# Kernel tuning notes

Hardware: AMD Instinct MI355X
Metric: run time of the kernel (lower is better)

## Reference

```python
import jax, jax.numpy as jnp
import numpy as np

N_HEAD = 16
N_EMBD = 1024
D_HEAD = N_EMBD // N_HEAD


def setup_inputs() -> dict:
    key = jax.random.key(0)
    ks = jax.random.split(key, 5)
    B, T, C = 4, 2048, N_EMBD
    s = 1.0 / np.sqrt(C)
    return {
        "x": jax.random.normal(ks[0], (B, T, C), dtype=jnp.float32),
        "w_qkv": jax.random.normal(ks[1], (C, 3 * C), dtype=jnp.float32) * s,
        "b_qkv": jnp.zeros((3 * C,), dtype=jnp.float32),
        "w_out": jax.random.normal(ks[2], (C, C), dtype=jnp.float32) * s,
        "b_out": jnp.zeros((C,), dtype=jnp.float32),
    }


def reference(x, w_qkv, b_qkv, w_out, b_out):
    B, T, C = x.shape
    qkv = x @ w_qkv + b_qkv  # [B,T,3C]
    q, k, v = jnp.split(qkv, 3, axis=-1)
    # [B,T,C] -> [B,H,T,D]
    def heads(t):
        return t.reshape(B, T, N_HEAD, D_HEAD).transpose(0, 2, 1, 3)
    q, k, v = heads(q), heads(k), heads(v)
    scores = jnp.einsum("bhqd,bhkd->bhqk", q, k) / np.sqrt(D_HEAD)
    causal = jnp.tril(jnp.ones((T, T), dtype=bool))
    scores = jnp.where(causal, scores, -jnp.inf)
    probs = jax.nn.softmax(scores, axis=-1)
    out = jnp.einsum("bhqk,bhkd->bhqd", probs, v)  # [B,H,T,D]
    out = out.transpose(0, 2, 1, 3).reshape(B, T, C)
    return out @ w_out + b_out
```

## Files before the change

### kernel.cpp

```cpp
#include <hip/hip_runtime.h>
#include <hip/hip_bf16.h>
#include <cstdint>
#include <cstddef>

typedef __attribute__((ext_vector_type(8))) short short8;
typedef __attribute__((ext_vector_type(4))) float f32x4;
typedef __attribute__((ext_vector_type(4))) uint16_t ushort4_t;

__device__ __forceinline__ uint16_t f2bf(float f) {
  union { float f; uint32_t u; } v; v.f = f;
  uint32_t r = v.u + 0x7FFFu + ((v.u >> 16) & 1u);
  return (uint16_t)(r >> 16);
}

__device__ __forceinline__ uint16_t f2bf_hw(float f) {
  union { __hip_bfloat16 h; uint16_t u; } cv;
  cv.h = __float2bfloat16(f);
  return cv.u;
}


__global__ __launch_bounds__(256) void cvt_f32_bf16(const float* __restrict__ in,
                                                    uint16_t* __restrict__ out, int n4) {
  int i = blockIdx.x * 256 + threadIdx.x;
  int stride = gridDim.x * 256;
  for (; i < n4; i += stride) {
    float4 v = ((const float4*)in)[i];
    ushort4_t o = { f2bf(v.x), f2bf(v.y), f2bf(v.z), f2bf(v.w) };
    ((ushort4_t*)out)[i] = o;
  }
}

__global__ __launch_bounds__(256) void transpose_cvt(const float* __restrict__ in,
                                                     uint16_t* __restrict__ out, int R, int C) {
  __shared__ float tile[32][33];
  int c0 = blockIdx.x * 32, r0 = blockIdx.y * 32;
  int tx = threadIdx.x, ty = threadIdx.y;
#pragma unroll
  for (int j = 0; j < 32; j += 8)
    tile[ty + j][tx] = in[(size_t)(r0 + ty + j) * C + c0 + tx];
  __syncthreads();
#pragma unroll
  for (int j = 0; j < 32; j += 8)
    out[(size_t)(c0 + ty + j) * R + r0 + tx] = f2bf(tile[tx][ty + j]);
}

__global__ __launch_bounds__(256) void transpose_v(const uint16_t* __restrict__ in,
                                                   uint16_t* __restrict__ out) {
  __shared__ uint16_t tile[32][33];
  int bh = blockIdx.z;
  int t0 = blockIdx.x * 32, d0 = blockIdx.y * 32;
  const uint16_t* ip = in + (size_t)bh * 2048 * 64;
  uint16_t* op = out + (size_t)bh * 64 * 2048;
  int tx = threadIdx.x, ty = threadIdx.y;
#pragma unroll
  for (int j = 0; j < 32; j += 8)
    tile[ty + j][tx] = ip[(size_t)(t0 + ty + j) * 64 + d0 + tx];
  __syncthreads();
#pragma unroll
  for (int j = 0; j < 32; j += 8)
    op[(size_t)(d0 + ty + j) * 2048 + t0 + tx] = tile[tx][ty + j];
}

__device__ __forceinline__ void stage16(const uint16_t* g, uint16_t* lds) {
  __builtin_amdgcn_global_load_lds((__attribute__((address_space(1))) void*)g,
                                   (__attribute__((address_space(3))) void*)lds, 16, 0, 0);
}

__global__ __launch_bounds__(256, 3) void gemm_qkv(
    const uint16_t* __restrict__ A, const uint16_t* __restrict__ Bt,
    const float* __restrict__ bias,
    uint16_t* __restrict__ q_out, uint16_t* __restrict__ k_out, uint16_t* __restrict__ v_out) {
  constexpr int K = 1024, KT = 16;
  __shared__ uint16_t lA[256 * 64];
  __shared__ uint16_t lB[128 * 64];
  const int tid = threadIdx.x;
  const int lane = tid & 63, w = tid >> 6;
  const int wm = w >> 1, wn = w & 1;
  const int r16 = lane & 15, hi = lane >> 4;
  const int wg = (blockIdx.x & 7) * 96 + (blockIdx.x >> 3);
  const int bm = wg / 24, bn = wg % 24;

  const int row0 = tid >> 3;
  const int cch0 = (tid & 7) ^ (row0 & 7);
  const uint16_t* aS = A + ((size_t)bm * 256 + row0) * K + cch0 * 8;
  const uint16_t* bS = Bt + ((size_t)bn * 128 + row0) * K + cch0 * 8;

  f32x4 acc[8][4];
#pragma unroll
  for (int m = 0; m < 8; ++m)
#pragma unroll
    for (int n = 0; n < 4; ++n) acc[m][n] = (f32x4){0.f, 0.f, 0.f, 0.f};

#pragma unroll 1
  for (int kt = 0; kt < KT; ++kt) {
#pragma unroll
    for (int it = 0; it < 8; ++it)
      stage16(aS + (size_t)(it * 32) * K + kt * 64, &lA[it * 2048 + tid * 8]);
#pragma unroll
    for (int it = 0; it < 4; ++it)
      stage16(bS + (size_t)(it * 32) * K + kt * 64, &lB[it * 2048 + tid * 8]);
    __syncthreads();

#pragma unroll
    for (int kk = 0; kk < 2; ++kk) {
      short8 bfr[4];
      const int swz = (kk * 64 + hi * 16) ^ ((r16 & 7) << 4);
#pragma unroll
      for (int n = 0; n < 4; ++n) {
        int rowb = wn * 64 + n * 16 + r16;
        bfr[n] = *(const short8*)((const char*)lB + rowb * 128 + swz);
      }
#pragma unroll
      for (int mh = 0; mh < 2; ++mh) {
        short8 af[4];
#pragma unroll
        for (int i = 0; i < 4; ++i) {
          int rowa = wm * 128 + mh * 64 + i * 16 + r16;
          af[i] = *(const short8*)((const char*)lA + rowa * 128 + swz);
        }
        __builtin_amdgcn_s_setprio(1);
#pragma unroll
        for (int i = 0; i < 4; ++i)
#pragma unroll
          for (int n = 0; n < 4; ++n)
            acc[mh * 4 + i][n] =
                __builtin_amdgcn_mfma_f32_16x16x32_bf16(af[i], bfr[n], acc[mh * 4 + i][n], 0, 0, 0);
        __builtin_amdgcn_s_setprio(0);
      }
    }
    __syncthreads();
  }

#pragma unroll
  for (int m = 0; m < 8; ++m) {
    int rg = bm * 256 + wm * 128 + (m >> 2) * 64 + (m & 3) * 16 + hi * 4;
#pragma unroll
    for (int n = 0; n < 4; ++n) {
      int cg = bn * 128 + wn * 64 + n * 16 + r16;
      float bv = bias[cg];
      int which = cg >> 10, hh = (cg >> 6) & 15, dd = cg & 63;
      uint16_t* dst = which == 0 ? q_out : (which == 1 ? k_out : v_out);
#pragma unroll
      for (int r = 0; r < 4; ++r) {
        int rgr = rg + r;
        dst[((size_t)((rgr >> 11) * 16 + hh) * 2048 + (rgr & 2047)) * 64 + dd] = f2bf(acc[m][n][r] + bv);
      }
    }
  }
}


__global__ __launch_bounds__(256) void gemm128_out(
    const uint16_t* __restrict__ A, const uint16_t* __restrict__ Bt,
    const float* __restrict__ bias, int K, float* __restrict__ f_out, int N) {
  __shared__ uint16_t lA[128 * 64];
  __shared__ uint16_t lB[128 * 64];
  const int tid = threadIdx.x;
  const int lane = tid & 63;
  const int w = tid >> 6, wm = w >> 1, wn = w & 1;
  const int r16 = lane & 15, hi = lane >> 4;
  const int bn = blockIdx.x, bm = blockIdx.y;

  f32x4 acc[4][4];
#pragma unroll
  for (int i = 0; i < 4; ++i)
#pragma unroll
    for (int j = 0; j < 4; ++j) acc[i][j] = (f32x4){0.f, 0.f, 0.f, 0.f};

  const int ksteps = K >> 6;
  for (int kt = 0; kt < ksteps; ++kt) {
#pragma unroll
    for (int it = 0; it < 4; ++it) {
      int ci = it * 256 + tid;
      int row = ci >> 3;
      int cch = (ci & 7) ^ (row & 7);
      stage16(A + (size_t)(bm * 128 + row) * K + kt * 64 + cch * 8, &lA[ci * 8]);
      stage16(Bt + (size_t)(bn * 128 + row) * K + kt * 64 + cch * 8, &lB[ci * 8]);
    }
    __syncthreads();
#pragma unroll
    for (int kk = 0; kk < 2; ++kk) {
      short8 af[4], bfr[4];
      int swz = (kk * 64 + hi * 16) ^ ((r16 & 7) << 4);
#pragma unroll
      for (int i = 0; i < 4; ++i) {
        int rowa = wm * 64 + i * 16 + r16;
        af[i] = *(const short8*)((const char*)lA + rowa * 128 + swz);
        int rowb = wn * 64 + i * 16 + r16;
        bfr[i] = *(const short8*)((const char*)lB + rowb * 128 + swz);
      }
#pragma unroll
      for (int i = 0; i < 4; ++i)
#pragma unroll
        for (int j = 0; j < 4; ++j)
          acc[i][j] = __builtin_amdgcn_mfma_f32_16x16x32_bf16(af[i], bfr[j], acc[i][j], 0, 0, 0);
    }
    __syncthreads();
  }

#pragma unroll
  for (int i = 0; i < 4; ++i) {
    int rbase = bm * 128 + wm * 64 + i * 16 + hi * 4;
#pragma unroll
    for (int j = 0; j < 4; ++j) {
      int cg = bn * 128 + wn * 64 + j * 16 + r16;
      float bv = bias[cg];
#pragma unroll
      for (int r = 0; r < 4; ++r)
        f_out[(size_t)(rbase + r) * N + cg] = acc[i][j][r] + bv;
    }
  }
}

__global__ __launch_bounds__(256, 3) void attn_fwd(
    const uint16_t* __restrict__ Qm, const uint16_t* __restrict__ Km,
    const uint16_t* __restrict__ Vt, uint16_t* __restrict__ O) {
  __shared__ uint16_t kbuf[2][64 * 64];
  __shared__ uint16_t vbuf[2][64 * 64];
  __shared__ uint16_t plds[4][32 * 72];
  const int tid = threadIdx.x;
  const int lane = tid & 63, w = tid >> 6;
  const int r16 = lane & 15, hi = lane >> 4;
  const int bid = blockIdx.x;
  const int bh = (bid & 7) + 8 * ((bid >> 3) & 7);
  const int qb = 15 - (bid >> 6);
  const int b = bh >> 4, h = bh & 15;
  const size_t base = (size_t)bh * 2048 * 64;
  const int qlo = qb * 128 + w * 32;
  const int NT = 2 * qb + 2;

  const float SC = 0.18033688011112042f;
  const float BIAS = -20.197730572445487f;

  short8 ones8;
#pragma unroll
  for (int i = 0; i < 8; ++i) ones8[i] = (short)0x3F80;

  short8 aq[2][2];
#pragma unroll
  for (int st = 0; st < 2; ++st)
#pragma unroll
    for (int c = 0; c < 2; ++c)
      aq[st][c] = *(const short8*)&Qm[base + (size_t)(qlo + st * 16 + r16) * 64 + c * 32 + hi * 8];

  f32x4 o[2][4];
  f32x4 o4[2];
#pragma unroll
  for (int st = 0; st < 2; ++st) {
#pragma unroll
    for (int j = 0; j < 4; ++j) o[st][j] = (f32x4){0.f, 0.f, 0.f, 0.f};
    o4[st] = (f32x4){0.f, 0.f, 0.f, 0.f};
  }

  auto stage_tile = [&](int pb, int kv0) {
    {
      int c = tid;            int row = c >> 3, cch = (c & 7) ^ (row & 7);
      stage16(Km + base + (size_t)(kv0 + row) * 64 + cch * 8, &kbuf[pb][c * 8]);
    }
    {
      int c = tid + 256;      int row = c >> 3, cch = (c & 7) ^ (row & 7);
      stage16(Km + base + (size_t)(kv0 + row) * 64 + cch * 8, &kbuf[pb][c * 8]);
    }
    {
      int c = tid;            int row = c >> 3, cch = (c & 7) ^ (row & 7);
      stage16(Vt + base + (size_t)row * 2048 + kv0 + cch * 8, &vbuf[pb][c * 8]);
    }
    {
      int c = tid + 256;      int row = c >> 3, cch = (c & 7) ^ (row & 7);
      stage16(Vt + base + (size_t)row * 2048 + kv0 + cch * 8, &vbuf[pb][c * 8]);
    }
  };

  int pb = 0;
  stage_tile(0, 0);
#pragma unroll 1
  for (int t = 0; t < NT; ++t) {
    const int kv0 = t << 6;
    if (t + 1 < NT) {
      stage_tile(pb ^ 1, (t + 1) << 6);
      asm volatile("s_waitcnt vmcnt(4)" ::: "memory");
    } else {
      asm volatile("s_waitcnt vmcnt(0)" ::: "memory");
    }
    __builtin_amdgcn_s_barrier();
    __builtin_amdgcn_sched_barrier(0);

    if (kv0 <= qlo + 31) {
      const bool maskt = (kv0 + 64 > qlo);
      short8 bk[4][2];
#pragma unroll
      for (int ct = 0; ct < 4; ++ct)
#pragma unroll
        for (int c = 0; c < 2; ++c) {
          int row = ct * 16 + r16;
          int ch = (c * 4 + hi) ^ (row & 7);
          bk[ct][c] = *(const short8*)((const char*)&kbuf[pb][0] + row * 128 + ch * 16);
        }

#pragma unroll
      for (int st = 0; st < 2; ++st) {
        f32x4 sc[4];
#pragma unroll
        for (int ct = 0; ct < 4; ++ct) sc[ct] = (f32x4){0.f, 0.f, 0.f, 0.f};
        __builtin_amdgcn_s_setprio(1);
#pragma unroll
        for (int ct = 0; ct < 4; ++ct)
#pragma unroll
          for (int c = 0; c < 2; ++c)
            sc[ct] = __builtin_amdgcn_mfma_f32_16x16x32_bf16(bk[ct][c], aq[st][c], sc[ct], 0, 0, 0);
        __builtin_amdgcn_s_setprio(0);

        uint16_t* pl = &plds[w][st * 16 * 72];
        const int qg = qlo + st * 16 + r16;
#pragma unroll
        for (int ct = 0; ct < 4; ++ct) {
          const int kb_ = kv0 + ct * 16 + hi * 4;
          float p0 = exp2f(fmaf(sc[ct][0], SC, BIAS));
          float p1 = exp2f(fmaf(sc[ct][1], SC, BIAS));
          float p2 = exp2f(fmaf(sc[ct][2], SC, BIAS));
          float p3 = exp2f(fmaf(sc[ct][3], SC, BIAS));
          if (maskt) {
            if (kb_ + 0 > qg) p0 = 0.f;
            if (kb_ + 1 > qg) p1 = 0.f;
            if (kb_ + 2 > qg) p2 = 0.f;
            if (kb_ + 3 > qg) p3 = 0.f;
          }
          ushort4_t pk4 = { f2bf_hw(p0), f2bf_hw(p1), f2bf_hw(p2), f2bf_hw(p3) };
          *(ushort4_t*)&pl[r16 * 72 + ct * 16 + hi * 4] = pk4;
        }
      }
      asm volatile("s_waitcnt lgkmcnt(0)" ::: "memory");
      __builtin_amdgcn_sched_barrier(0);

      short8 ap[2][2];
#pragma unroll
      for (int st = 0; st < 2; ++st)
#pragma unroll
        for (int ks = 0; ks < 2; ++ks)
          ap[st][ks] = *(const short8*)&plds[w][(st * 16 + r16) * 72 + ks * 32 + hi * 8];
      short8 bv[4][2];
#pragma unroll
      for (int j = 0; j < 4; ++j)
#pragma unroll
        for (int ks = 0; ks < 2; ++ks) {
          int row = j * 16 + r16;
          int ch = (ks * 4 + hi) ^ (row & 7);
          bv[j][ks] = *(const short8*)((const char*)&vbuf[pb][0] + row * 128 + ch * 16);
        }
      __builtin_amdgcn_s_setprio(1);
#pragma unroll
      for (int st = 0; st < 2; ++st) {
#pragma unroll
        for (int ks = 0; ks < 2; ++ks)
          o4[st] = __builtin_amdgcn_mfma_f32_16x16x32_bf16(ones8, ap[st][ks], o4[st], 0, 0, 0);
#pragma unroll
        for (int j = 0; j < 4; ++j)
#pragma unroll
          for (int ks = 0; ks < 2; ++ks)
            o[st][j] = __builtin_amdgcn_mfma_f32_16x16x32_bf16(bv[j][ks], ap[st][ks], o[st][j], 0, 0, 0);
      }
      __builtin_amdgcn_s_setprio(0);
    }

    __builtin_amdgcn_s_barrier();
    __builtin_amdgcn_sched_barrier(0);
    pb ^= 1;
  }

#pragma unroll
  for (int st = 0; st < 2; ++st) {
    float inv = 1.f / o4[st][0];
    int qg = qlo + st * 16 + r16;
    size_t rowo = ((size_t)(b * 2048 + qg)) * 1024 + h * 64;
#pragma unroll
    for (int j = 0; j < 4; ++j) {
      ushort4_t v4 = { f2bf(o[st][j][0] * inv), f2bf(o[st][j][1] * inv),
                       f2bf(o[st][j][2] * inv), f2bf(o[st][j][3] * inv) };
      *(ushort4_t*)&O[rowo + j * 16 + hi * 4] = v4;
    }
  }
}


extern "C" void kernel_launch(void* const* d_in, const int* in_sizes, int n_in,
                              void* d_out, int out_size, void* d_ws, size_t ws_size,
                              hipStream_t stream) {
  const float* x = (const float*)d_in[0];
  const float* w_qkv = (const float*)d_in[1];
  const float* b_qkv = (const float*)d_in[2];
  const float* w_out = (const float*)d_in[3];
  const float* b_out = (const float*)d_in[4];
  float* out = (float*)d_out;

  const size_t BT = 8192, C = 1024, N3 = 3072, BHTD = 8388608;
  char* p = (char*)d_ws;
  uint16_t* xbf = (uint16_t*)p;   p += BT * C * 2;
  uint16_t* wqkvT = (uint16_t*)p; p += N3 * C * 2;
  uint16_t* woutT = (uint16_t*)p; p += C * C * 2;
  uint16_t* qb = (uint16_t*)p;    p += BHTD * 2;
  uint16_t* kb = (uint16_t*)p;    p += BHTD * 2;
  uint16_t* vb = (uint16_t*)p;    p += BHTD * 2;
  uint16_t* vtb = (uint16_t*)p;   p += BHTD * 2;
  uint16_t* ob = (uint16_t*)p;    p += BHTD * 2;

  cvt_f32_bf16<<<2048, 256, 0, stream>>>(x, xbf, (int)(BT * C / 4));
  transpose_cvt<<<dim3(96, 32), dim3(32, 8), 0, stream>>>(w_qkv, wqkvT, 1024, 3072);
  transpose_cvt<<<dim3(32, 32), dim3(32, 8), 0, stream>>>(w_out, woutT, 1024, 1024);
  gemm_qkv<<<768, 256, 0, stream>>>(xbf, wqkvT, b_qkv, qb, kb, vb);
  transpose_v<<<dim3(64, 2, 64), dim3(32, 8), 0, stream>>>(vb, vtb);
  attn_fwd<<<1024, 256, 0, stream>>>(qb, kb, vtb, ob);
  gemm128_out<<<dim3(8, 64), 256, 0, stream>>>(ob, woutT, b_out, 1024, out, 1024);
}
```

Before: 182.8 us.

## Switch attention to 32x32 MFMA with register-resident P, dropping LDS round trip

Rewrites the attention inner loop to use 32x32x16 bf16 MFMA tiles so the score accumulator layout feeds straight into the PV MFMA as the B operand. This removes the per-wave P scratch buffer in LDS, its write/wait/read round trip, and the ones-vector MFMA used for the row sum, which is now computed with VALU adds plus one cross-half shuffle at the end. It also uses a packed bf16 convert instruction and raises the occupancy hint to 4 blocks per CU. In exchange, V is read from LDS with smaller 8-byte loads, and register pressure may rise under the tighter launch bound.

```diff
diff --git a/kernel.cpp b/kernel.cpp
--- a/kernel.cpp
+++ b/kernel.cpp
@@ -5,18 +5,15 @@
 
 typedef __attribute__((ext_vector_type(8))) short short8;
 typedef __attribute__((ext_vector_type(4))) float f32x4;
+typedef __attribute__((ext_vector_type(16))) float f32x16;
 typedef __attribute__((ext_vector_type(4))) uint16_t ushort4_t;
+typedef __attribute__((ext_vector_type(4))) uint32_t uint4_t;
+typedef __attribute__((ext_vector_type(2))) uint32_t uint2_t;
 
 __device__ __forceinline__ uint16_t f2bf(float f) {
   union { float f; uint32_t u; } v; v.f = f;
   uint32_t r = v.u + 0x7FFFu + ((v.u >> 16) & 1u);
   return (uint16_t)(r >> 16);
-}
-
-__device__ __forceinline__ uint16_t f2bf_hw(float f) {
-  union { __hip_bfloat16 h; uint16_t u; } cv;
-  cv.h = __float2bfloat16(f);
-  return cv.u;
 }
 
 
@@ -213,15 +210,14 @@
   }
 }
 
-__global__ __launch_bounds__(256, 3) void attn_fwd(
+__global__ __launch_bounds__(256, 4) void attn_fwd(
     const uint16_t* __restrict__ Qm, const uint16_t* __restrict__ Km,
     const uint16_t* __restrict__ Vt, uint16_t* __restrict__ O) {
   __shared__ uint16_t kbuf[2][64 * 64];
   __shared__ uint16_t vbuf[2][64 * 64];
-  __shared__ uint16_t plds[4][32 * 72];
   const int tid = threadIdx.x;
   const int lane = tid & 63, w = tid >> 6;
-  const int r16 = lane & 15, hi = lane >> 4;
+  const int l31 = lane & 31, h2 = lane >> 5;
   const int bid = blockIdx.x;
   const int bh = (bid & 7) + 8 * ((bid >> 3) & 7);
   const int qb = 15 - (bid >> 6);
@@ -229,29 +225,20 @@
   const size_t base = (size_t)bh * 2048 * 64;
   const int qlo = qb * 128 + w * 32;
   const int NT = 2 * qb + 2;
+  const int qg = qlo + l31;
 
   const float SC = 0.18033688011112042f;
   const float BIAS = -20.197730572445487f;
 
-  short8 ones8;
-#pragma unroll
-  for (int i = 0; i < 8; ++i) ones8[i] = (short)0x3F80;
-
-  short8 aq[2][2];
-#pragma unroll
-  for (int st = 0; st < 2; ++st)
-#pragma unroll
-    for (int c = 0; c < 2; ++c)
-      aq[st][c] = *(const short8*)&Qm[base + (size_t)(qlo + st * 16 + r16) * 64 + c * 32 + hi * 8];
-
-  f32x4 o[2][4];
-  f32x4 o4[2];
-#pragma unroll
-  for (int st = 0; st < 2; ++st) {
-#pragma unroll
-    for (int j = 0; j < 4; ++j) o[st][j] = (f32x4){0.f, 0.f, 0.f, 0.f};
-    o4[st] = (f32x4){0.f, 0.f, 0.f, 0.f};
-  }
+  short8 aq[4];
+#pragma unroll
+  for (int dk = 0; dk < 4; ++dk)
+    aq[dk] = *(const short8*)&Qm[base + (size_t)qg * 64 + dk * 16 + h2 * 8];
+
+  f32x16 o[2];
+  float lsum = 0.f;
+#pragma unroll
+  for (int i = 0; i < 16; ++i) { o[0][i] = 0.f; o[1][i] = 0.f; }
 
   auto stage_tile = [&](int pb, int kv0) {
     {
@@ -288,79 +275,61 @@
 
     if (kv0 <= qlo + 31) {
       const bool maskt = (kv0 + 64 > qlo);
-      short8 bk[4][2];
-#pragma unroll
-      for (int ct = 0; ct < 4; ++ct)
-#pragma unroll
-        for (int c = 0; c < 2; ++c) {
-          int row = ct * 16 + r16;
-          int ch = (c * 4 + hi) ^ (row & 7);
-          bk[ct][c] = *(const short8*)((const char*)&kbuf[pb][0] + row * 128 + ch * 16);
+#pragma unroll
+      for (int ct = 0; ct < 2; ++ct) {
+        f32x16 sc;
+#pragma unroll
+        for (int i = 0; i < 16; ++i) sc[i] = 0.f;
+        __builtin_amdgcn_s_setprio(1);
+#pragma unroll
+        for (int dk = 0; dk < 4; ++dk) {
+          int row = ct * 32 + l31;
+          int ch = (dk * 2 + h2) ^ (row & 7);
+          short8 bk = *(const short8*)((const char*)&kbuf[pb][0] + row * 128 + ch * 16);
+          sc = __builtin_amdgcn_mfma_f32_32x32x16_bf16(bk, aq[dk], sc, 0, 0, 0);
         }
-
-#pragma unroll
-      for (int st = 0; st < 2; ++st) {
-        f32x4 sc[4];
-#pragma unroll
-        for (int ct = 0; ct < 4; ++ct) sc[ct] = (f32x4){0.f, 0.f, 0.f, 0.f};
+        __builtin_amdgcn_s_setprio(0);
+
+        float p[16];
+        const int kb0 = kv0 + ct * 32 + 4 * h2;
+#pragma unroll
+        for (int r = 0; r < 16; ++r) {
+          const int cr = (r & 3) + 8 * (r >> 2);
+          float x = exp2f(fmaf(sc[r], SC, BIAS));
+          if (maskt && (kb0 + cr > qg)) x = 0.f;
+          p[r] = x;
+        }
+        lsum += (((p[0] + p[1]) + (p[2] + p[3])) + ((p[4] + p[5]) + (p[6] + p[7])))
+              + (((p[8] + p[9]) + (p[10] + p[11])) + ((p[12] + p[13]) + (p[14] + p[15])));
+
+        short8 pf[2];
+#pragma unroll
+        for (int kc = 0; kc < 2; ++kc) {
+          uint32_t d0, d1, d2, d3;
+          asm("v_cvt_pk_bf16_f32 %0, %1, %2" : "=v"(d0) : "v"(p[8 * kc + 0]), "v"(p[8 * kc + 1]));
+          asm("v_cvt_pk_bf16_f32 %0, %1, %2" : "=v"(d1) : "v"(p[8 * kc + 2]), "v"(p[8 * kc + 3]));
+          asm("v_cvt_pk_bf16_f32 %0, %1, %2" : "=v"(d2) : "v"(p[8 * kc + 4]), "v"(p[8 * kc + 5]));
+          asm("v_cvt_pk_bf16_f32 %0, %1, %2" : "=v"(d3) : "v"(p[8 * kc + 6]), "v"(p[8 * kc + 7]));
+          uint4_t uu = { d0, d1, d2, d3 };
+          pf[kc] = __builtin_bit_cast(short8, uu);
+        }
+
         __builtin_amdgcn_s_setprio(1);
 #pragma unroll
-        for (int ct = 0; ct < 4; ++ct)
-#pragma unroll
-          for (int c = 0; c < 2; ++c)
-            sc[ct] = __builtin_amdgcn_mfma_f32_16x16x32_bf16(bk[ct][c], aq[st][c], sc[ct], 0, 0, 0);
+        for (int dt = 0; dt < 2; ++dt)
+#pragma unroll
+          for (int kc = 0; kc < 2; ++kc) {
+            int row = dt * 32 + l31;
+            int c0 = (((ct * 4 + kc * 2 + 0) ^ (row & 7)) << 4) + h2 * 8;
+            int c1 = (((ct * 4 + kc * 2 + 1) ^ (row & 7)) << 4) + h2 * 8;
+            uint2_t vlo = *(const uint2_t*)((const char*)&vbuf[pb][0] + row * 128 + c0);
+            uint2_t vhi = *(const uint2_t*)((const char*)&vbuf[pb][0] + row * 128 + c1);
+            uint4_t uu = { vlo[0], vlo[1], vhi[0], vhi[1] };
+            short8 bv = __builtin_bit_cast(short8, uu);
+            o[dt] = __builtin_amdgcn_mfma_f32_32x32x16_bf16(bv, pf[kc], o[dt], 0, 0, 0);
+          }
         __builtin_amdgcn_s_setprio(0);
-
-        uint16_t* pl = &plds[w][st * 16 * 72];
-        const int qg = qlo + st * 16 + r16;
-#pragma unroll
-        for (int ct = 0; ct < 4; ++ct) {
-          const int kb_ = kv0 + ct * 16 + hi * 4;
-          float p0 = exp2f(fmaf(sc[ct][0], SC, BIAS));
-          float p1 = exp2f(fmaf(sc[ct][1], SC, BIAS));
-          float p2 = exp2f(fmaf(sc[ct][2], SC, BIAS));
-          float p3 = exp2f(fmaf(sc[ct][3], SC, BIAS));
-          if (maskt) {
-            if (kb_ + 0 > qg) p0 = 0.f;
-            if (kb_ + 1 > qg) p1 = 0.f;
-            if (kb_ + 2 > qg) p2 = 0.f;
-            if (kb_ + 3 > qg) p3 = 0.f;
-          }
-          ushort4_t pk4 = { f2bf_hw(p0), f2bf_hw(p1), f2bf_hw(p2), f2bf_hw(p3) };
-          *(ushort4_t*)&pl[r16 * 72 + ct * 16 + hi * 4] = pk4;
-        }
-      }
-      asm volatile("s_waitcnt lgkmcnt(0)" ::: "memory");
-      __builtin_amdgcn_sched_barrier(0);
-
-      short8 ap[2][2];
-#pragma unroll
-      for (int st = 0; st < 2; ++st)
-#pragma unroll
-        for (int ks = 0; ks < 2; ++ks)
-          ap[st][ks] = *(const short8*)&plds[w][(st * 16 + r16) * 72 + ks * 32 + hi * 8];
-      short8 bv[4][2];
-#pragma unroll
-      for (int j = 0; j < 4; ++j)
-#pragma unroll
-        for (int ks = 0; ks < 2; ++ks) {
-          int row = j * 16 + r16;
-          int ch = (ks * 4 + hi) ^ (row & 7);
-          bv[j][ks] = *(const short8*)((const char*)&vbuf[pb][0] + row * 128 + ch * 16);
-        }
-      __builtin_amdgcn_s_setprio(1);
-#pragma unroll
-      for (int st = 0; st < 2; ++st) {
-#pragma unroll
-        for (int ks = 0; ks < 2; ++ks)
-          o4[st] = __builtin_amdgcn_mfma_f32_16x16x32_bf16(ones8, ap[st][ks], o4[st], 0, 0, 0);
-#pragma unroll
-        for (int j = 0; j < 4; ++j)
-#pragma unroll
-          for (int ks = 0; ks < 2; ++ks)
-            o[st][j] = __builtin_amdgcn_mfma_f32_16x16x32_bf16(bv[j][ks], ap[st][ks], o[st][j], 0, 0, 0);
-      }
-      __builtin_amdgcn_s_setprio(0);
+      }
     }
 
     __builtin_amdgcn_s_barrier();
@@ -368,17 +337,19 @@
     pb ^= 1;
   }
 
-#pragma unroll
-  for (int st = 0; st < 2; ++st) {
-    float inv = 1.f / o4[st][0];
-    int qg = qlo + st * 16 + r16;
+  {
+    float lt = lsum + __shfl_xor(lsum, 32, 64);
+    float inv = 1.f / lt;
     size_t rowo = ((size_t)(b * 2048 + qg)) * 1024 + h * 64;
 #pragma unroll
-    for (int j = 0; j < 4; ++j) {
-      ushort4_t v4 = { f2bf(o[st][j][0] * inv), f2bf(o[st][j][1] * inv),
-                       f2bf(o[st][j][2] * inv), f2bf(o[st][j][3] * inv) };
-      *(ushort4_t*)&O[rowo + j * 16 + hi * 4] = v4;
-    }
+    for (int dt = 0; dt < 2; ++dt)
+#pragma unroll
+      for (int rq = 0; rq < 4; ++rq) {
+        int d = dt * 32 + 8 * rq + 4 * h2;
+        ushort4_t v4 = { f2bf(o[dt][4 * rq + 0] * inv), f2bf(o[dt][4 * rq + 1] * inv),
+                         f2bf(o[dt][4 * rq + 2] * inv), f2bf(o[dt][4 * rq + 3] * inv) };
+        *(ushort4_t*)&O[rowo + d] = v4;
+      }
   }
 }
 
```

Result: slower. 207.6 us (+13.6%).

## Keep softmax probabilities in registers and permute V reads to match MFMA layout

Applied to the files above, without the earlier changes.

Removes the per-wave LDS staging buffer for the probability tile. Scores are now packed to bf16 in registers with v_cvt_pk_bf16_f32 and fed straight into the PV MFMAs, and the V operand loads are rearranged so its k-index ordering matches the register layout of P. This drops LDS writes, reads and a waitcnt/sched barrier per tile, and frees LDS so launch bounds can go from 3 to 4 blocks per CU. In exchange V is read with twice as many smaller 8-byte LDS loads, and the denser occupancy target may push register pressure up.

```diff
diff --git a/kernel.cpp b/kernel.cpp
--- a/kernel.cpp
+++ b/kernel.cpp
@@ -6,17 +6,13 @@
 typedef __attribute__((ext_vector_type(8))) short short8;
 typedef __attribute__((ext_vector_type(4))) float f32x4;
 typedef __attribute__((ext_vector_type(4))) uint16_t ushort4_t;
+typedef __attribute__((ext_vector_type(4))) uint32_t uint4_t;
+typedef __attribute__((ext_vector_type(2))) uint32_t uint2_t;
 
 __device__ __forceinline__ uint16_t f2bf(float f) {
   union { float f; uint32_t u; } v; v.f = f;
   uint32_t r = v.u + 0x7FFFu + ((v.u >> 16) & 1u);
   return (uint16_t)(r >> 16);
-}
-
-__device__ __forceinline__ uint16_t f2bf_hw(float f) {
-  union { __hip_bfloat16 h; uint16_t u; } cv;
-  cv.h = __float2bfloat16(f);
-  return cv.u;
 }
 
 
@@ -213,12 +209,11 @@
   }
 }
 
-__global__ __launch_bounds__(256, 3) void attn_fwd(
+__global__ __launch_bounds__(256, 4) void attn_fwd(
     const uint16_t* __restrict__ Qm, const uint16_t* __restrict__ Km,
     const uint16_t* __restrict__ Vt, uint16_t* __restrict__ O) {
   __shared__ uint16_t kbuf[2][64 * 64];
   __shared__ uint16_t vbuf[2][64 * 64];
-  __shared__ uint16_t plds[4][32 * 72];
   const int tid = threadIdx.x;
   const int lane = tid & 63, w = tid >> 6;
   const int r16 = lane & 15, hi = lane >> 4;
@@ -311,56 +306,50 @@
             sc[ct] = __builtin_amdgcn_mfma_f32_16x16x32_bf16(bk[ct][c], aq[st][c], sc[ct], 0, 0, 0);
         __builtin_amdgcn_s_setprio(0);
 
-        uint16_t* pl = &plds[w][st * 16 * 72];
+        float p[4][4];
         const int qg = qlo + st * 16 + r16;
 #pragma unroll
         for (int ct = 0; ct < 4; ++ct) {
           const int kb_ = kv0 + ct * 16 + hi * 4;
-          float p0 = exp2f(fmaf(sc[ct][0], SC, BIAS));
-          float p1 = exp2f(fmaf(sc[ct][1], SC, BIAS));
-          float p2 = exp2f(fmaf(sc[ct][2], SC, BIAS));
-          float p3 = exp2f(fmaf(sc[ct][3], SC, BIAS));
-          if (maskt) {
-            if (kb_ + 0 > qg) p0 = 0.f;
-            if (kb_ + 1 > qg) p1 = 0.f;
-            if (kb_ + 2 > qg) p2 = 0.f;
-            if (kb_ + 3 > qg) p3 = 0.f;
+#pragma unroll
+          for (int r = 0; r < 4; ++r) {
+            float x = exp2f(fmaf(sc[ct][r], SC, BIAS));
+            if (maskt && (kb_ + r > qg)) x = 0.f;
+            p[ct][r] = x;
           }
-          ushort4_t pk4 = { f2bf_hw(p0), f2bf_hw(p1), f2bf_hw(p2), f2bf_hw(p3) };
-          *(ushort4_t*)&pl[r16 * 72 + ct * 16 + hi * 4] = pk4;
         }
+
+        short8 pf[2];
+#pragma unroll
+        for (int ks = 0; ks < 2; ++ks) {
+          uint32_t d0, d1, d2, d3;
+          asm("v_cvt_pk_bf16_f32 %0, %1, %2" : "=v"(d0) : "v"(p[2 * ks][0]), "v"(p[2 * ks][1]));
+          asm("v_cvt_pk_bf16_f32 %0, %1, %2" : "=v"(d1) : "v"(p[2 * ks][2]), "v"(p[2 * ks][3]));
+          asm("v_cvt_pk_bf16_f32 %0, %1, %2" : "=v"(d2) : "v"(p[2 * ks + 1][0]), "v"(p[2 * ks + 1][1]));
+          asm("v_cvt_pk_bf16_f32 %0, %1, %2" : "=v"(d3) : "v"(p[2 * ks + 1][2]), "v"(p[2 * ks + 1][3]));
+          uint4_t uu = { d0, d1, d2, d3 };
+          pf[ks] = __builtin_bit_cast(short8, uu);
+        }
+
+        __builtin_amdgcn_s_setprio(1);
+#pragma unroll
+        for (int ks = 0; ks < 2; ++ks)
+          o4[st] = __builtin_amdgcn_mfma_f32_16x16x32_bf16(ones8, pf[ks], o4[st], 0, 0, 0);
+#pragma unroll
+        for (int j = 0; j < 4; ++j)
+#pragma unroll
+          for (int ks = 0; ks < 2; ++ks) {
+            int row = j * 16 + r16;
+            int c0 = (((ks * 4 + (hi >> 1)) ^ (row & 7)) << 4) + (hi & 1) * 8;
+            int c1 = (((ks * 4 + 2 + (hi >> 1)) ^ (row & 7)) << 4) + (hi & 1) * 8;
+            uint2_t vlo = *(const uint2_t*)((const char*)&vbuf[pb][0] + row * 128 + c0);
+            uint2_t vhi = *(const uint2_t*)((const char*)&vbuf[pb][0] + row * 128 + c1);
+            uint4_t uu = { vlo[0], vlo[1], vhi[0], vhi[1] };
+            short8 bv = __builtin_bit_cast(short8, uu);
+            o[st][j] = __builtin_amdgcn_mfma_f32_16x16x32_bf16(bv, pf[ks], o[st][j], 0, 0, 0);
+          }
+        __builtin_amdgcn_s_setprio(0);
       }
-      asm volatile("s_waitcnt lgkmcnt(0)" ::: "memory");
-      __builtin_amdgcn_sched_barrier(0);
-
-      short8 ap[2][2];
-#pragma unroll
-      for (int st = 0; st < 2; ++st)
-#pragma unroll
-        for (int ks = 0; ks < 2; ++ks)
-          ap[st][ks] = *(const short8*)&plds[w][(st * 16 + r16) * 72 + ks * 32 + hi * 8];
-      short8 bv[4][2];
-#pragma unroll
-      for (int j = 0; j < 4; ++j)
-#pragma unroll
-        for (int ks = 0; ks < 2; ++ks) {
-          int row = j * 16 + r16;
-          int ch = (ks * 4 + hi) ^ (row & 7);
-          bv[j][ks] = *(const short8*)((const char*)&vbuf[pb][0] + row * 128 + ch * 16);
-        }
-      __builtin_amdgcn_s_setprio(1);
-#pragma unroll
-      for (int st = 0; st < 2; ++st) {
-#pragma unroll
-        for (int ks = 0; ks < 2; ++ks)
-          o4[st] = __builtin_amdgcn_mfma_f32_16x16x32_bf16(ones8, ap[st][ks], o4[st], 0, 0, 0);
-#pragma unroll
-        for (int j = 0; j < 4; ++j)
-#pragma unroll
-          for (int ks = 0; ks < 2; ++ks)
-            o[st][j] = __builtin_amdgcn_mfma_f32_16x16x32_bf16(bv[j][ks], ap[st][ks], o[st][j], 0, 0, 0);
-      }
-      __builtin_amdgcn_s_setprio(0);
     }
 
     __builtin_amdgcn_s_barrier();
```

New measurement: 297.5 us. +62.7%, slower.
